# Kernel tuning notes

Hardware: AMD Instinct MI355X
Metric: run time of the kernel (lower is better)

Reference implementation:

```python
import jax, jax.numpy as jnp
import numpy as np

N = 50000          # nodes
E = 800000         # edges
D_IN = 64          # env INPUT_DIM
D_H = 64           # env HIDDEN_DIM
D_OUT = 32         # env OUTPUT_DIM
A_H = 16           # action HIDDEN_DIM
NUM_ENV = 3        # env NUM_LAYERS
TAU = 1.0          # gumbel temperature (fixed, LEARN_TEMPERATURE=False)
LN_EPS = 1e-5


def setup_inputs() -> dict:
    key = jax.random.key(0)
    ks = jax.random.split(key, 24)

    def lin(k, fan_in, fan_out):
        s = 1.0 / np.sqrt(fan_in)
        kw, kb = jax.random.split(k)
        W = jax.random.uniform(kw, (fan_in, fan_out), jnp.float32, -s, s)
        b = jax.random.uniform(kb, (fan_out,), jnp.float32, -s, s)
        return W, b

    inp = {}
    inp['x'] = jax.random.normal(ks[0], (N, D_IN), jnp.float32)
    inp['edge_index'] = jax.random.randint(ks[1], (2, E), 0, N, dtype=jnp.int32)

    inp['W_enc'], inp['b_enc'] = lin(ks[2], D_IN, D_H)
    env_W, env_b = [], []
    for l in range(NUM_ENV):
        W, b = lin(ks[3 + l], 2 * D_H, D_H)
        env_W.append(W); env_b.append(b)
    inp['env_W'] = jnp.stack(env_W)   # [NUM_ENV, 2*D_H, D_H]
    inp['env_b'] = jnp.stack(env_b)   # [NUM_ENV, D_H]
    inp['W_dec'], inp['b_dec'] = lin(ks[6], D_H, D_OUT)
    inp['ln_g'] = jnp.ones((D_H,), jnp.float32)
    inp['ln_b'] = jnp.zeros((D_H,), jnp.float32)
    inp['in_W1'], inp['in_b1'] = lin(ks[7], 2 * D_H, A_H)
    inp['in_W2'], inp['in_b2'] = lin(ks[8], 2 * A_H, 2)
    inp['out_W1'], inp['out_b1'] = lin(ks[9], 2 * D_H, A_H)
    inp['out_W2'], inp['out_b2'] = lin(ks[10], 2 * A_H, 2)
    return inp


def _layernorm(x, g, b):
    mu = jnp.mean(x, axis=-1, keepdims=True)
    var = jnp.var(x, axis=-1, keepdims=True)
    return (x - mu) * jax.lax.rsqrt(var + LN_EPS) * g + b


def _conv(x, src, dst, W, b, edge_weight=None):
    # WeightedGNNConv: gather x[src] -> (optional * edge_weight) -> scatter-add at dst -> lin(concat(x, agg))
    msg = x[src]                                   # [E, d]
    if edge_weight is not None:
        msg = msg * edge_weight[:, None]
    agg = jax.ops.segment_sum(msg, dst, num_segments=N)
    return jnp.concatenate([x, agg], axis=-1) @ W + b


def _action_net(x, src, dst, W1, b1, W2, b2):
    h = jax.nn.relu(_conv(x, src, dst, W1, b1))
    return _conv(h, src, dst, W2, b2)              # [N, 2] logits


def _gumbel_hard(logits, key, tau):
    u = jax.random.uniform(key, logits.shape, logits.dtype, 1e-20, 1.0)
    g = -jnp.log(-jnp.log(u))
    y = jax.nn.softmax((logits + g) / tau, axis=-1)
    y_hard = jax.nn.one_hot(jnp.argmax(y, axis=-1), logits.shape[-1], dtype=y.dtype)
    return y + jax.lax.stop_gradient(y_hard - y)   # straight-through


def reference(x, edge_index, W_enc, b_enc, env_W, env_b, W_dec, b_dec, ln_g, ln_b,
              in_W1, in_b1, in_W2, in_b2, out_W1, out_b1, out_W2, out_b2):
    src, dst = edge_index[0], edge_index[1]        # u, v
    h = x @ W_enc + b_enc                          # encoder (dropout is identity in eval)
    noise_key = jax.random.key(1234)
    ews = []
    for l in range(NUM_ENV):
        h = _layernorm(h, ln_g, ln_b)
        in_logits = _action_net(h, src, dst, in_W1, in_b1, in_W2, in_b2)
        out_logits = _action_net(h, src, dst, out_W1, out_b1, out_W2, out_b2)
        in_p = _gumbel_hard(in_logits, jax.random.fold_in(noise_key, 2 * l), TAU)
        out_p = _gumbel_hard(out_logits, jax.random.fold_in(noise_key, 2 * l + 1), TAU)
        # create_edge_weight: keep_in_prob[v] * keep_out_prob[u]
        ew = in_p[:, 0][dst] * out_p[:, 0][src]    # [E], values in {0,1}
        ews.append(ew)
        h = _conv(h, src, dst, env_W[l], env_b[l], edge_weight=ew)
    out = h @ W_dec + b_dec
    return out, jnp.stack(ews)
```

## Files before the change

kernel.cpp:

```cpp
#include <hip/hip_runtime.h>
#include <math.h>

static constexpr int NN = 50000;
static constexpr int EE = 800000;

typedef unsigned long long ull;

struct TF2 { unsigned a, b; };

__host__ __device__ __forceinline__ TF2 tf2x32(unsigned k0, unsigned k1,
                                               unsigned x0, unsigned x1) {
  unsigned k2 = k0 ^ k1 ^ 0x1BD11BDAu;
  x0 += k0; x1 += k1;
#define TFR(r) { x0 += x1; x1 = (x1 << (r)) | (x1 >> (32 - (r))); x1 ^= x0; }
  TFR(13) TFR(15) TFR(26) TFR(6)
  x0 += k1; x1 += k2 + 1u;
  TFR(17) TFR(29) TFR(16) TFR(24)
  x0 += k2; x1 += k0 + 2u;
  TFR(13) TFR(15) TFR(26) TFR(6)
  x0 += k0; x1 += k1 + 3u;
  TFR(17) TFR(29) TFR(16) TFR(24)
  x0 += k1; x1 += k2 + 4u;
  TFR(13) TFR(15) TFR(26) TFR(6)
  x0 += k2; x1 += k0 + 5u;
#undef TFR
  TF2 r; r.a = x0; r.b = x1; return r;
}

__device__ __forceinline__ float u01_bits(unsigned w) {
  float fl = __uint_as_float((w >> 9) | 0x3f800000u) - 1.0f;
  return fmaxf(1e-20f, fl + 1e-20f);
}

__device__ __forceinline__ float keep01(float l0, float l1, unsigned k0, unsigned k1, int node) {
  unsigned f0 = 2u * (unsigned)node, f1 = f0 + 1u;
  TF2 t0 = tf2x32(k0, k1, 0u, f0);
  TF2 t1 = tf2x32(k0, k1, 0u, f1);
  float g0 = -logf(-logf(u01_bits(t0.a ^ t0.b)));
  float g1 = -logf(-logf(u01_bits(t1.a ^ t1.b)));
  float z0 = l0 + g0, z1 = l1 + g1;
  float m  = fmaxf(z0, z1);
  float e0 = expf(z0 - m), e1 = expf(z1 - m);
  float s  = e0 + e1;
  float y0 = e0 / s, y1 = e1 / s;
  return (y1 > y0) ? 0.0f : 1.0f;
}

__global__ void k_count(const int* __restrict__ dst, int* __restrict__ deg, int e) {
  int i = blockIdx.x * blockDim.x + threadIdx.x;
  if (i < e) atomicAdd(&deg[dst[i]], 1);
}

__global__ void k_bsum(const int* __restrict__ deg, int* __restrict__ bsum, int n) {
  int i = blockIdx.x * 256 + threadIdx.x;
  int v = (i < n) ? deg[i] : 0;
  #pragma unroll
  for (int off = 32; off; off >>= 1) v += __shfl_xor(v, off, 64);
  __shared__ int ws[4];
  if ((threadIdx.x & 63) == 0) ws[threadIdx.x >> 6] = v;
  __syncthreads();
  if (threadIdx.x == 0) bsum[blockIdx.x] = ws[0] + ws[1] + ws[2] + ws[3];
}

__global__ void k_bscan(const int* __restrict__ bsum, int* __restrict__ bpref,
                        int nb, int* __restrict__ row_ptr, int n) {
  __shared__ int s[256];
  int t = threadIdx.x;
  int v = (t < nb) ? bsum[t] : 0;
  s[t] = v; __syncthreads();
  for (int off = 1; off < 256; off <<= 1) {
    int u = (t >= off) ? s[t - off] : 0;
    __syncthreads();
    s[t] += u;
    __syncthreads();
  }
  bpref[t] = s[t] - v;
  if (t == 0) row_ptr[n] = s[255];
}

__global__ void k_prefix(const int* __restrict__ deg, const int* __restrict__ bpref,
                         int* __restrict__ row_ptr, int* __restrict__ cursor, int n) {
  __shared__ int s[256];
  int t = threadIdx.x;
  int i = blockIdx.x * 256 + t;
  int v = (i < n) ? deg[i] : 0;
  s[t] = v; __syncthreads();
  for (int off = 1; off < 256; off <<= 1) {
    int u = (t >= off) ? s[t - off] : 0;
    __syncthreads();
    s[t] += u;
    __syncthreads();
  }
  if (i < n) {
    int ex = s[t] - v + bpref[blockIdx.x];
    row_ptr[i] = ex; cursor[i] = ex;
  }
}

__global__ void k_fill(const int* __restrict__ src, const int* __restrict__ dst,
                       int* __restrict__ cursor, ull* __restrict__ ce, int e) {
  int i = blockIdx.x * blockDim.x + threadIdx.x;
  if (i < e) {
    int pos = atomicAdd(&cursor[dst[i]], 1);
    ce[pos] = ((ull)(unsigned)src[i] << 20) | (unsigned)i;
  }
}

__global__ void k_enc_ln(const float* __restrict__ x, const float* __restrict__ W,
                         const float* __restrict__ bias, const float* __restrict__ g,
                         const float* __restrict__ bb, float* __restrict__ hln) {
  __shared__ float Ws[64 * 64];
  for (int i = threadIdx.x; i < 64 * 64; i += 256) Ws[i] = W[i];
  __syncthreads();
  int node = blockIdx.x * 4 + (threadIdx.x >> 6);
  int j = threadIdx.x & 63;
  const float* xr = x + (size_t)node * 64;
  float s = bias[j];
  #pragma unroll
  for (int i = 0; i < 64; i++) s = fmaf(xr[i], Ws[i * 64 + j], s);
  float t = s;
  #pragma unroll
  for (int off = 32; off; off >>= 1) t += __shfl_xor(t, off, 64);
  float mu = t * (1.0f / 64.0f);
  float d = s - mu;
  float q = d * d;
  #pragma unroll
  for (int off = 32; off; off >>= 1) q += __shfl_xor(q, off, 64);
  float rs = 1.0f / sqrtf(q * (1.0f / 64.0f) + 1e-5f);
  hln[(size_t)node * 64 + j] = d * rs * g[j] + bb[j];
}

__global__ void k_proj(const float* __restrict__ hln,
                       const float* __restrict__ W1i, const float* __restrict__ W1o,
                       float* __restrict__ P1, float* __restrict__ S1, int nchunk) {
  int t = threadIdx.x, w = t >> 6, lane = t & 63;
  int h = lane >> 5, jo = lane & 31;
  const float* Wg = (jo < 16) ? W1i : W1o;
  int col = jo & 15;
  float wr[64];
  #pragma unroll
  for (int i = 0; i < 64; i++) wr[i] = Wg[(h * 64 + i) * 16 + col];
  __shared__ float st[256];
  for (int blk = blockIdx.x; blk < nchunk; blk += gridDim.x) {
    __syncthreads();
    st[t] = hln[(size_t)blk * 256 + t];
    __syncthreads();
    const float* sv = &st[w * 64];
    float a = 0.f;
    #pragma unroll
    for (int i = 0; i < 64; i++) a = fmaf(sv[i], wr[i], a);
    size_t node = (size_t)blk * 4 + w;
    if (h == 0) S1[node * 32 + jo] = a;
    else        P1[node * 32 + jo] = a;
  }
}

__global__ void k_gatherA(const float* __restrict__ P1, const float* __restrict__ S1,
                          const int* __restrict__ row_ptr, const ull* __restrict__ ce,
                          const float* __restrict__ inb1, const float* __restrict__ outb1,
                          const float* __restrict__ inW2, const float* __restrict__ outW2,
                          float* __restrict__ P2S2) {
  int t = threadIdx.x;
  int w = t >> 6, lane = t & 63;
  int sub = lane >> 5, j = lane & 31;
  int node = blockIdx.x * 8 + w * 2 + sub;
  int b = row_ptr[node], e = row_ptr[node + 1];
  float s0 = 0.f, s1 = 0.f;
  for (int base = b; base < e; base += 32) {
    int idx = base + j;
    int u_l = (idx < e) ? (int)(ce[idx] >> 20) : 0;
    int cnt = min(32, e - base);
    int k = 0;
    for (; k + 2 <= cnt; k += 2) {
      int u0 = __shfl(u_l, k, 32), u1 = __shfl(u_l, k + 1, 32);
      s0 += P1[(size_t)u0 * 32 + j];
      s1 += P1[(size_t)u1 * 32 + j];
    }
    if (k < cnt) s0 += P1[(size_t)__shfl(u_l, k, 32) * 32 + j];
  }
  float agg = s0 + s1;
  float b1j = (j < 16) ? inb1[j] : outb1[j - 16];
  float rj = fmaxf(S1[(size_t)node * 32 + j] + agg + b1j, 0.f);
  float wa0, wa1, wb0, wb1;
  if (j < 16) {
    wa0 = inW2[j * 2 + 0];  wa1 = inW2[j * 2 + 1];
    wb0 = inW2[(16 + j) * 2 + 0];  wb1 = inW2[(16 + j) * 2 + 1];
  } else {
    int j2 = j - 16;
    wa0 = outW2[j2 * 2 + 0];  wa1 = outW2[j2 * 2 + 1];
    wb0 = outW2[(16 + j2) * 2 + 0];  wb1 = outW2[(16 + j2) * 2 + 1];
  }
  float v0 = rj * wa0, v1 = rj * wa1, v2 = rj * wb0, v3 = rj * wb1;
  #pragma unroll
  for (int off = 8; off; off >>= 1) {
    v0 += __shfl_xor(v0, off, 64);
    v1 += __shfl_xor(v1, off, 64);
    v2 += __shfl_xor(v2, off, 64);
    v3 += __shfl_xor(v3, off, 64);
  }
  float* row = P2S2 + (size_t)node * 8;
  if (j == 0)  { row[0] = v2; row[1] = v3; row[4] = v0; row[5] = v1; }
  if (j == 16) { row[2] = v2; row[3] = v3; row[6] = v0; row[7] = v1; }
}

__global__ void k_gatherB(const float* __restrict__ P2S2, const int* __restrict__ row_ptr,
                          const ull* __restrict__ ce,
                          const float* __restrict__ inb2, const float* __restrict__ outb2,
                          float* __restrict__ keep_in, float* __restrict__ keep_out,
                          unsigned ki0, unsigned ki1, unsigned ko0, unsigned ko1) {
  int t = threadIdx.x;
  int w = t >> 6, lane = t & 63;
  int g = lane >> 4, el = lane & 15;
  int node = blockIdx.x * 16 + w * 4 + g;
  int b = row_ptr[node], e = row_ptr[node + 1];
  float a0 = 0.f, a1 = 0.f, a2 = 0.f, a3 = 0.f;
  for (int base = b; base < e; base += 16) {
    int idx = base + el;
    if (idx < e) {
      int u = (int)(ce[idx] >> 20);
      float4 p = *(const float4*)(P2S2 + (size_t)u * 8);
      a0 += p.x; a1 += p.y; a2 += p.z; a3 += p.w;
    }
  }
  #pragma unroll
  for (int off = 8; off; off >>= 1) {
    a0 += __shfl_xor(a0, off, 64);
    a1 += __shfl_xor(a1, off, 64);
    a2 += __shfl_xor(a2, off, 64);
    a3 += __shfl_xor(a3, off, 64);
  }
  float4 sf = *(const float4*)(P2S2 + (size_t)node * 8 + 4);
  if (el == 0)
    keep_in[node]  = keep01(sf.x + a0 + inb2[0],  sf.y + a1 + inb2[1],  ki0, ki1, node);
  else if (el == 1)
    keep_out[node] = keep01(sf.z + a2 + outb2[0], sf.w + a3 + outb2[1], ko0, ko1, node);
}

template <bool LN>
__global__ void k_aggC(const float* __restrict__ hln, const int* __restrict__ row_ptr,
                       const ull* __restrict__ ce, const float* __restrict__ keep_in,
                       const float* __restrict__ keep_out, float* __restrict__ ew,
                       const float* __restrict__ W, const float* __restrict__ bias,
                       const float* __restrict__ g, const float* __restrict__ bb,
                       float* __restrict__ hout) {
  __shared__ float Ws[128 * 64];
  __shared__ __align__(16) float st[4][128];
  int t = threadIdx.x;
  for (int i = t; i < 128 * 64; i += 256) Ws[i] = W[i];
  __syncthreads();
  int w = t >> 6, lane = t & 63;
  int node = blockIdx.x * 4 + w;
  float ki = keep_in[node];
  float hv = hln[(size_t)node * 64 + lane];
  int b = row_ptr[node], e = row_ptr[node + 1];
  float s0 = 0.f, s1 = 0.f, s2 = 0.f, s3 = 0.f;
  for (int base = b; base < e; base += 64) {
    int idx = base + lane;
    int u_l = 0; float ko_l = 0.f;
    if (idx < e) {
      ull c = ce[idx];
      u_l = (int)(c >> 20);
      ko_l = keep_out[u_l];
      ew[(unsigned)(c & 0xFFFFFu)] = ki * ko_l;
    }
    if (ki != 0.f) {
      int cnt = min(64, e - base);
      int k = 0;
      for (; k + 4 <= cnt; k += 4) {
        int u0 = __shfl(u_l, k, 64),     u1 = __shfl(u_l, k + 1, 64),
            u2 = __shfl(u_l, k + 2, 64), u3 = __shfl(u_l, k + 3, 64);
        float w0 = __shfl(ko_l, k, 64),     w1 = __shfl(ko_l, k + 1, 64),
              w2 = __shfl(ko_l, k + 2, 64), w3 = __shfl(ko_l, k + 3, 64);
        if (w0 != 0.f) s0 += hln[(size_t)u0 * 64 + lane];
        if (w1 != 0.f) s1 += hln[(size_t)u1 * 64 + lane];
        if (w2 != 0.f) s2 += hln[(size_t)u2 * 64 + lane];
        if (w3 != 0.f) s3 += hln[(size_t)u3 * 64 + lane];
      }
      for (; k < cnt; k++) {
        int u0 = __shfl(u_l, k, 64);
        float w0 = __shfl(ko_l, k, 64);
        if (w0 != 0.f) s0 += hln[(size_t)u0 * 64 + lane];
      }
    }
  }
  float s = ((s0 + s1) + (s2 + s3)) * ki;
  st[w][lane]      = hv;
  st[w][64 + lane] = s;
  float a0 = bias[lane], a1 = 0.f, a2 = 0.f, a3 = 0.f;
  #pragma unroll 4
  for (int i = 0; i < 128; i += 4) {
    float4 c4 = *(const float4*)(&st[w][i]);
    a0 = fmaf(c4.x, Ws[(i    ) * 64 + lane], a0);
    a1 = fmaf(c4.y, Ws[(i + 1) * 64 + lane], a1);
    a2 = fmaf(c4.z, Ws[(i + 2) * 64 + lane], a2);
    a3 = fmaf(c4.w, Ws[(i + 3) * 64 + lane], a3);
  }
  float acc = (a0 + a1) + (a2 + a3);
  if (LN) {
    float tt = acc;
    #pragma unroll
    for (int off = 32; off; off >>= 1) tt += __shfl_xor(tt, off, 64);
    float mu = tt * (1.0f / 64.0f);
    float d = acc - mu;
    float q = d * d;
    #pragma unroll
    for (int off = 32; off; off >>= 1) q += __shfl_xor(q, off, 64);
    float rs = 1.0f / sqrtf(q * (1.0f / 64.0f) + 1e-5f);
    hout[(size_t)node * 64 + lane] = d * rs * g[lane] + bb[lane];
  } else {
    hout[(size_t)node * 64 + lane] = acc;
  }
}

__global__ void k_dec(const float* __restrict__ h, const float* __restrict__ W,
                      const float* __restrict__ bias, float* __restrict__ out) {
  __shared__ float Ws[64 * 32];
  int t = threadIdx.x;
  for (int i = t; i < 64 * 32; i += 256) Ws[i] = W[i];
  __syncthreads();
  int node = blockIdx.x * 8 + (t >> 5);
  int j = t & 31;
  const float* hr = h + (size_t)node * 64;
  float s = bias[j];
  #pragma unroll
  for (int i = 0; i < 64; i++) s = fmaf(hr[i], Ws[i * 32 + j], s);
  out[(size_t)node * 32 + j] = s;
}

extern "C" void kernel_launch(void* const* d_in, const int* in_sizes, int n_in,
                              void* d_out, int out_size, void* d_ws, size_t ws_size,
                              hipStream_t stream) {
  const float* x      = (const float*)d_in[0];
  const int*   ei     = (const int*)  d_in[1];
  const float* W_enc  = (const float*)d_in[2];
  const float* b_enc  = (const float*)d_in[3];
  const float* env_W  = (const float*)d_in[4];
  const float* env_b  = (const float*)d_in[5];
  const float* W_dec  = (const float*)d_in[6];
  const float* b_dec  = (const float*)d_in[7];
  const float* ln_g   = (const float*)d_in[8];
  const float* ln_b   = (const float*)d_in[9];
  const float* in_W1  = (const float*)d_in[10];
  const float* in_b1  = (const float*)d_in[11];
  const float* in_W2  = (const float*)d_in[12];
  const float* in_b2  = (const float*)d_in[13];
  const float* out_W1 = (const float*)d_in[14];
  const float* out_b1 = (const float*)d_in[15];
  const float* out_W2 = (const float*)d_in[16];
  const float* out_b2 = (const float*)d_in[17];

  const int n = NN, e = EE;
  const int* src = ei;
  const int* dst = ei + e;

  float* out_h  = (float*)d_out;
  float* out_ew = out_h + (size_t)n * 32;

  size_t off = 0;
  auto alloc = [&](size_t bytes) -> void* {
    void* p = (char*)d_ws + off;
    off += (bytes + 255) & ~(size_t)255;
    return p;
  };
  float* hlnA    = (float*)alloc((size_t)n * 64 * 4);
  float* hlnB    = (float*)alloc((size_t)n * 64 * 4);
  float* P1      = (float*)alloc((size_t)n * 32 * 4);
  float* S1      = (float*)alloc((size_t)n * 32 * 4);
  float* P2S2    = (float*)alloc((size_t)n * 8 * 4);
  float* keep_i  = (float*)alloc((size_t)n * 4);
  float* keep_o  = (float*)alloc((size_t)n * 4);
  int*   deg     = (int*)alloc((size_t)n * 4);
  int*   row_ptr = (int*)alloc((size_t)(n + 1) * 4);
  int*   cursor  = (int*)alloc((size_t)n * 4);
  int*   bsum    = (int*)alloc(256 * 4);
  int*   bpref   = (int*)alloc(256 * 4);
  ull*   ce      = (ull*)alloc((size_t)e * 8);
  if (off > ws_size) return;

  const int nb = (n + 255) / 256;

  hipMemsetAsync(deg, 0, (size_t)n * 4, stream);
  k_count<<<(e + 255) / 256, 256, 0, stream>>>(dst, deg, e);
  k_bsum<<<nb, 256, 0, stream>>>(deg, bsum, n);
  k_bscan<<<1, 256, 0, stream>>>(bsum, bpref, nb, row_ptr, n);
  k_prefix<<<nb, 256, 0, stream>>>(deg, bpref, row_ptr, cursor, n);
  k_fill<<<(e + 255) / 256, 256, 0, stream>>>(src, dst, cursor, ce, e);

  const int g4  = n / 4;
  const int g8  = n / 8;
  const int g16 = n / 16;

  k_enc_ln<<<g4, 256, 0, stream>>>(x, W_enc, b_enc, ln_g, ln_b, hlnA);

  float* hln = hlnA;
  float* hln_next = hlnB;
  for (int l = 0; l < 3; l++) {
    TF2 kin  = tf2x32(0u, 1234u, 0u, (unsigned)(2 * l));
    TF2 kout = tf2x32(0u, 1234u, 0u, (unsigned)(2 * l + 1));

    k_proj<<<1250, 256, 0, stream>>>(hln, in_W1, out_W1, P1, S1, g4);
    k_gatherA<<<g8, 256, 0, stream>>>(P1, S1, row_ptr, ce, in_b1, out_b1,
                                      in_W2, out_W2, P2S2);
    k_gatherB<<<g16, 256, 0, stream>>>(P2S2, row_ptr, ce, in_b2, out_b2,
                                       keep_i, keep_o, kin.a, kin.b, kout.a, kout.b);
    if (l < 2) {
      k_aggC<true><<<g4, 256, 0, stream>>>(hln, row_ptr, ce, keep_i, keep_o,
                                           out_ew + (size_t)l * e,
                                           env_W + (size_t)l * 128 * 64,
                                           env_b + (size_t)l * 64, ln_g, ln_b, hln_next);
    } else {
      k_aggC<false><<<g4, 256, 0, stream>>>(hln, row_ptr, ce, keep_i, keep_o,
                                            out_ew + (size_t)l * e,
                                            env_W + (size_t)l * 128 * 64,
                                            env_b + (size_t)l * 64, ln_g, ln_b, hln_next);
    }
    float* tmp = hln; hln = hln_next; hln_next = tmp;
  }

  k_dec<<<g8, 256, 0, stream>>>(hln, W_dec, b_dec, out_h);
}
```

Measured before the change: 708.2 us.

## Precompute env-layer linear projections before edge aggregation in a separate kernel

The env conv's linear layer is split algebraically: a new projection kernel computes h@W_top+b and h@W_bot per node, and the aggregation kernel then sums projected neighbour rows and adds the top part, instead of aggregating raw features and running a 128x64 matvec per node. This removes the per-block 32KB weight load into shared memory and the per-node matmul from the gather kernel, which should raise its occupancy. In exchange it adds a kernel launch and writes and reads two extra N x 64 buffers. Floating-point summation order also changes slightly.

```diff
diff --git a/kernel.cpp b/kernel.cpp
--- a/kernel.cpp
+++ b/kernel.cpp
@@ -155,6 +155,33 @@
   }
 }
 
+__global__ void k_projE(const float* __restrict__ hln, const float* __restrict__ W,
+                        const float* __restrict__ bias,
+                        float* __restrict__ Htop, float* __restrict__ Pbot, int nchunk) {
+  __shared__ float Ws[128 * 64];
+  __shared__ float st[256];
+  int t = threadIdx.x;
+  for (int i = t; i < 128 * 64; i += 256) Ws[i] = W[i];
+  int w = t >> 6, lane = t & 63;
+  float bj = bias[lane];
+  for (int blk = blockIdx.x; blk < nchunk; blk += gridDim.x) {
+    __syncthreads();
+    st[t] = hln[(size_t)blk * 256 + t];
+    __syncthreads();
+    const float* sv = &st[w * 64];
+    float a = bj, b = 0.f;
+    #pragma unroll
+    for (int i = 0; i < 64; i++) {
+      float hv = sv[i];
+      a = fmaf(hv, Ws[i * 64 + lane], a);
+      b = fmaf(hv, Ws[(64 + i) * 64 + lane], b);
+    }
+    size_t node = (size_t)blk * 4 + w;
+    Htop[node * 64 + lane] = a;
+    Pbot[node * 64 + lane] = b;
+  }
+}
+
 __global__ void k_gatherA(const float* __restrict__ P1, const float* __restrict__ S1,
                           const int* __restrict__ row_ptr, const ull* __restrict__ ce,
                           const float* __restrict__ inb1, const float* __restrict__ outb1,
@@ -237,21 +264,15 @@
 }
 
 template <bool LN>
-__global__ void k_aggC(const float* __restrict__ hln, const int* __restrict__ row_ptr,
-                       const ull* __restrict__ ce, const float* __restrict__ keep_in,
-                       const float* __restrict__ keep_out, float* __restrict__ ew,
-                       const float* __restrict__ W, const float* __restrict__ bias,
-                       const float* __restrict__ g, const float* __restrict__ bb,
-                       float* __restrict__ hout) {
-  __shared__ float Ws[128 * 64];
-  __shared__ __align__(16) float st[4][128];
-  int t = threadIdx.x;
-  for (int i = t; i < 128 * 64; i += 256) Ws[i] = W[i];
-  __syncthreads();
+__global__ void k_aggD(const float* __restrict__ Htop, const float* __restrict__ Pbot,
+                       const int* __restrict__ row_ptr, const ull* __restrict__ ce,
+                       const float* __restrict__ keep_in, const float* __restrict__ keep_out,
+                       float* __restrict__ ew, const float* __restrict__ g,
+                       const float* __restrict__ bb, float* __restrict__ hout) {
+  int t = threadIdx.x;
   int w = t >> 6, lane = t & 63;
   int node = blockIdx.x * 4 + w;
   float ki = keep_in[node];
-  float hv = hln[(size_t)node * 64 + lane];
   int b = row_ptr[node], e = row_ptr[node + 1];
   float s0 = 0.f, s1 = 0.f, s2 = 0.f, s3 = 0.f;
   for (int base = b; base < e; base += 64) {
@@ -271,31 +292,19 @@
             u2 = __shfl(u_l, k + 2, 64), u3 = __shfl(u_l, k + 3, 64);
         float w0 = __shfl(ko_l, k, 64),     w1 = __shfl(ko_l, k + 1, 64),
               w2 = __shfl(ko_l, k + 2, 64), w3 = __shfl(ko_l, k + 3, 64);
-        if (w0 != 0.f) s0 += hln[(size_t)u0 * 64 + lane];
-        if (w1 != 0.f) s1 += hln[(size_t)u1 * 64 + lane];
-        if (w2 != 0.f) s2 += hln[(size_t)u2 * 64 + lane];
-        if (w3 != 0.f) s3 += hln[(size_t)u3 * 64 + lane];
+        if (w0 != 0.f) s0 += Pbot[(size_t)u0 * 64 + lane];
+        if (w1 != 0.f) s1 += Pbot[(size_t)u1 * 64 + lane];
+        if (w2 != 0.f) s2 += Pbot[(size_t)u2 * 64 + lane];
+        if (w3 != 0.f) s3 += Pbot[(size_t)u3 * 64 + lane];
       }
       for (; k < cnt; k++) {
         int u0 = __shfl(u_l, k, 64);
         float w0 = __shfl(ko_l, k, 64);
-        if (w0 != 0.f) s0 += hln[(size_t)u0 * 64 + lane];
+        if (w0 != 0.f) s0 += Pbot[(size_t)u0 * 64 + lane];
       }
     }
   }
-  float s = ((s0 + s1) + (s2 + s3)) * ki;
-  st[w][lane]      = hv;
-  st[w][64 + lane] = s;
-  float a0 = bias[lane], a1 = 0.f, a2 = 0.f, a3 = 0.f;
-  #pragma unroll 4
-  for (int i = 0; i < 128; i += 4) {
-    float4 c4 = *(const float4*)(&st[w][i]);
-    a0 = fmaf(c4.x, Ws[(i    ) * 64 + lane], a0);
-    a1 = fmaf(c4.y, Ws[(i + 1) * 64 + lane], a1);
-    a2 = fmaf(c4.z, Ws[(i + 2) * 64 + lane], a2);
-    a3 = fmaf(c4.w, Ws[(i + 3) * 64 + lane], a3);
-  }
-  float acc = (a0 + a1) + (a2 + a3);
+  float acc = Htop[(size_t)node * 64 + lane] + ((s0 + s1) + (s2 + s3)) * ki;
   if (LN) {
     float tt = acc;
     #pragma unroll
@@ -364,6 +373,8 @@
   };
   float* hlnA    = (float*)alloc((size_t)n * 64 * 4);
   float* hlnB    = (float*)alloc((size_t)n * 64 * 4);
+  float* Htop    = (float*)alloc((size_t)n * 64 * 4);
+  float* Pbot    = (float*)alloc((size_t)n * 64 * 4);
   float* P1      = (float*)alloc((size_t)n * 32 * 4);
   float* S1      = (float*)alloc((size_t)n * 32 * 4);
   float* P2S2    = (float*)alloc((size_t)n * 8 * 4);
@@ -398,21 +409,19 @@
     TF2 kin  = tf2x32(0u, 1234u, 0u, (unsigned)(2 * l));
     TF2 kout = tf2x32(0u, 1234u, 0u, (unsigned)(2 * l + 1));
 
+    k_projE<<<1250, 256, 0, stream>>>(hln, env_W + (size_t)l * 128 * 64,
+                                      env_b + (size_t)l * 64, Htop, Pbot, g4);
     k_proj<<<1250, 256, 0, stream>>>(hln, in_W1, out_W1, P1, S1, g4);
     k_gatherA<<<g8, 256, 0, stream>>>(P1, S1, row_ptr, ce, in_b1, out_b1,
                                       in_W2, out_W2, P2S2);
     k_gatherB<<<g16, 256, 0, stream>>>(P2S2, row_ptr, ce, in_b2, out_b2,
                                        keep_i, keep_o, kin.a, kin.b, kout.a, kout.b);
     if (l < 2) {
-      k_aggC<true><<<g4, 256, 0, stream>>>(hln, row_ptr, ce, keep_i, keep_o,
-                                           out_ew + (size_t)l * e,
-                                           env_W + (size_t)l * 128 * 64,
-                                           env_b + (size_t)l * 64, ln_g, ln_b, hln_next);
+      k_aggD<true><<<g4, 256, 0, stream>>>(Htop, Pbot, row_ptr, ce, keep_i, keep_o,
+                                           out_ew + (size_t)l * e, ln_g, ln_b, hln_next);
     } else {
-      k_aggC<false><<<g4, 256, 0, stream>>>(hln, row_ptr, ce, keep_i, keep_o,
-                                            out_ew + (size_t)l * e,
-                                            env_W + (size_t)l * 128 * 64,
-                                            env_b + (size_t)l * 64, ln_g, ln_b, hln_next);
+      k_aggD<false><<<g4, 256, 0, stream>>>(Htop, Pbot, row_ptr, ce, keep_i, keep_o,
+                                            out_ew + (size_t)l * e, ln_g, ln_b, hln_next);
     }
     float* tmp = hln; hln = hln_next; hln_next = tmp;
   }
```

Measured after the change: 643.0 us. 1.1x faster.
